# Kernel tuning notes

Measured on AMD Instinct MI355X. Metric: run time of the kernel, lower is better.

## Reference

```python
import jax, jax.numpy as jnp
import numpy as np

B, L, D = 16, 4096, 512


def setup_inputs() -> dict:
    key = jax.random.key(0)
    ks = jax.random.split(key, 8)
    s = 1.0 / np.sqrt(D)
    x = jax.random.normal(ks[0], (B, L, D), dtype=jnp.float32)
    Wk = jax.random.normal(ks[1], (D, D), dtype=jnp.float32) * s
    Wq = jax.random.normal(ks[2], (D, D), dtype=jnp.float32) * s
    Wv = jax.random.normal(ks[3], (D, D), dtype=jnp.float32) * s
    bk = jnp.zeros((D,), jnp.float32)
    bq = jnp.zeros((D,), jnp.float32)
    bv = jnp.zeros((D,), jnp.float32)
    lens = jax.random.randint(ks[4], (B,), 1, L + 1, dtype=jnp.int32)
    return {"x": x, "Wk": Wk, "bk": bk, "Wq": Wq, "bq": bq,
            "Wv": Wv, "bv": bv, "lens": lens}


def reference(x, Wk, bk, Wq, bq, Wv, bv, lens):
    # Dropout is identity in eval mode.
    x_k = jnp.tanh(jnp.einsum('bld,ed->ble', x, Wk) + bk)  # [B,L,D]
    x_q = jnp.tanh(jnp.einsum('bld,ed->ble', x, Wq) + bq)
    x_v = jnp.tanh(jnp.einsum('bld,ed->ble', x, Wv) + bv)
    # sum_j (x_k_i . x_q_j) == x_k_i . sum_j x_q_j  (algebraic collapse of the L x L bmm)
    q_sum = x_q.sum(axis=1)                                # [B,D]
    w = jnp.einsum('bld,bd->bl', x_k, q_sum) / (D ** 0.5)  # [B,L]
    pad = jnp.arange(L)[None, :] >= lens[:, None]          # True at padding
    w = jnp.where(pad, -jnp.inf, w)
    w = jax.nn.softmax(w, axis=1)                          # [B,L]
    # (x_v * w[...,None]).sum(-1) == x_v.sum(-1) * w
    return x_v.sum(axis=-1) * w                            # [B,L]
```

## Files before the change

kernel.cpp:

```cpp
#include <hip/hip_runtime.h>
#include <hip/hip_bf16.h>

typedef __attribute__((ext_vector_type(4)))  int   i32x4;
typedef __attribute__((ext_vector_type(16))) int   i32x16;
typedef __attribute__((ext_vector_type(16))) float f32x16;
typedef __attribute__((ext_vector_type(8)))  short short8;

#define SC1 (1.0f/4096.0f)
#define SC2 (1.0f/524288.0f)

static __device__ __forceinline__ float ftanh(float x) {
  float e = __builtin_amdgcn_exp2f(x * 2.885390081777927f);
  return 1.0f - 2.0f * __builtin_amdgcn_rcpf(e + 1.0f);
}
static __device__ __forceinline__ unsigned short bf16_rn(float f) {
  unsigned u = __float_as_uint(f);
  u += 0x7FFFu + ((u >> 16) & 1u);
  return (unsigned short)(u >> 16);
}
static __device__ __forceinline__ void quant2(float x, float sc, float inv, float losc,
                                              int& hi, int& lo) {
  float t  = __builtin_fmaf(x, sc, 12582912.0f);
  hi = __float_as_int(t) - 0x4B400000;
  float hf = t - 12582912.0f;
  float r  = __builtin_fmaf(hf, -inv, x);
  float t2 = __builtin_fmaf(r, losc, 12582912.0f);
  lo = __float_as_int(t2) - 0x4B400000;
}
static __device__ __forceinline__ void gll16(const void* g, void* l) {
  __builtin_amdgcn_global_load_lds((const __attribute__((address_space(1))) unsigned int*)g,
                                   (__attribute__((address_space(3))) unsigned int*)l, 16, 0, 0);
}
#define MFMA_I8(ACC, A, B) \
  asm("v_mfma_i32_32x32x32_i8 %0, %1, %2, %0" : "+v"(ACC) : "v"(A), "v"(B))

__global__ void prep_w(const float* __restrict__ Wq, const float* __restrict__ Wk,
                       const float* __restrict__ Wv,
                       char* __restrict__ B1, char* __restrict__ B2) {
  int gid = blockIdx.x * 256 + threadIdx.x;
  if (gid < 65536) {
    int chunk = gid >> 12, g = gid & 4095;
    char* dst = B1 + chunk * 65536 + g * 16;
    if (g < 2048) {
      int sel = g >> 10;
      int gg = g & 1023, nt = gg >> 6, lane = gg & 63;
      const float* src = Wq + (size_t)(nt * 32 + (lane & 31)) * 512 + chunk * 32 + (lane >> 5) * 16;
      union { char b[16]; i32x4 v; } ob;
#pragma unroll
      for (int j = 0; j < 16; ++j) {
        int h, l; quant2(src[j], 256.f, 1.f / 256.f, 32768.f, h, l);
        ob.b[j] = (char)(sel ? l : h);
      }
      *(i32x4*)dst = ob.v;
    } else {
      int gg = g - 2048, nt = gg >> 7, ks = (gg >> 6) & 1, lane = gg & 63;
      const float* src = Wv + (size_t)(nt * 32 + (lane & 31)) * 512 + chunk * 32 + ks * 16 + (lane >> 5) * 8;
      union { unsigned short s[8]; i32x4 v; } ob;
#pragma unroll
      for (int j = 0; j < 8; ++j) ob.s[j] = bf16_rn(src[j]);
      *(i32x4*)dst = ob.v;
    }
  } else {
    int gid2 = gid - 65536;
    int chunk = gid2 >> 11, g = gid2 & 2047;
    char* dst = B2 + chunk * 32768 + g * 16;
    int sel = g >> 10, gg = g & 1023, nt = gg >> 6, lane = gg & 63;
    const float* src = Wk + (size_t)(nt * 32 + (lane & 31)) * 512 + chunk * 32 + (lane >> 5) * 16;
    union { char b[16]; i32x4 v; } ob;
#pragma unroll
    for (int j = 0; j < 16; ++j) {
      int h, l; quant2(src[j], 256.f, 1.f / 256.f, 32768.f, h, l);
      ob.b[j] = (char)(sel ? l : h);
    }
    *(i32x4*)dst = ob.v;
  }
}

template<bool VBF16>
static __device__ __forceinline__ void stageA(char* Ab, int tid, float4 xv) {
  const int row = tid >> 3, d0 = (tid & 7) * 4;
  const int mt = row >> 5, l31 = row & 31;
  int h0, l0, h1, l1, h2, l2, h3, l3;
  quant2(xv.x, 16.f, 0.0625f, 2048.f, h0, l0);
  quant2(xv.y, 16.f, 0.0625f, 2048.f, h1, l1);
  quant2(xv.z, 16.f, 0.0625f, 2048.f, h2, l2);
  quant2(xv.w, 16.f, 0.0625f, 2048.f, h3, l3);
  unsigned wh = (h0 & 255) | ((h1 & 255) << 8) | ((h2 & 255) << 16) | ((unsigned)(h3 & 255) << 24);
  unsigned wl = (l0 & 255) | ((l1 & 255) << 8) | ((l2 & 255) << 16) | ((unsigned)(l3 & 255) << 24);
  const int lane8 = (d0 >> 4) * 32 + l31, j = d0 & 15;
  *(unsigned*)(Ab + (mt * 64 + lane8) * 16 + j) = wh;
  *(unsigned*)(Ab + 2048 + (mt * 64 + lane8) * 16 + j) = wl;
  if (VBF16) {
    unsigned long long b0 = bf16_rn(xv.x), b1 = bf16_rn(xv.y), b2 = bf16_rn(xv.z), b3 = bf16_rn(xv.w);
    unsigned long long vv = b0 | (b1 << 16) | (b2 << 32) | (b3 << 48);
    const int ks = d0 >> 4, rem = d0 & 15, hs8 = rem >> 3, j8 = rem & 7;
    *(unsigned long long*)(Ab + 4096 + ((mt * 2 + ks) * 64 + hs8 * 32 + l31) * 16 + j8 * 2) = vv;
  }
}

__global__ __launch_bounds__(512, 2) void pass1_qv(
    const float* __restrict__ x, const char* __restrict__ B1,
    const float* __restrict__ bq, const float* __restrict__ bv,
    float* __restrict__ qpart, float* __restrict__ svout) {
  extern __shared__ char smem[];
  char* Bb0 = smem;            char* Bb1 = smem + 65536;
  char* Ab0 = smem + 131072;   char* Ab1 = smem + 139264;
  float* redv = (float*)(smem + 147456);

  const int tid = threadIdx.x, lane = tid & 63, w = tid >> 6;
  const int l31 = lane & 31, hs = lane >> 5;
  const float* xrow = x + ((size_t)blockIdx.x * 64 + (tid >> 3)) * 512 + (tid & 7) * 4;

  i32x16 q1[2][2] = {}; i32x16 q2[2][2] = {};
  f32x16 accv[2][2] = {};

  float4 xcur = *(const float4*)(xrow);
  stageA<true>(Ab0, tid, xcur);
  {
    const char* src = B1 + tid * 16;
    char* dst = Bb0 + tid * 16;
#pragma unroll
    for (int i = 0; i < 8; ++i) gll16(src + i * 8192, dst + i * 8192);
  }
  xcur = *(const float4*)(xrow + 32);

#pragma unroll 1
  for (int c = 0; c < 16; ++c) {
    const int p = c & 1;
    char* Bc = p ? Bb1 : Bb0;  char* Bn = p ? Bb0 : Bb1;
    char* Ac = p ? Ab1 : Ab0;  char* An = p ? Ab0 : Ab1;
    __syncthreads();
    if (c < 15) {
      const char* src = B1 + (size_t)(c + 1) * 65536 + tid * 16;
      char* dst = Bn + tid * 16;
#pragma unroll
      for (int i = 0; i < 8; ++i) gll16(src + i * 8192, dst + i * 8192);
    }
    float4 xnext = xcur;
    if (c < 14) xnext = *(const float4*)(xrow + (c + 2) * 32);
    if (c < 15) stageA<true>(An, tid, xcur);

    const int lo16 = lane * 16;
    i32x4 aqh0 = *(const i32x4*)(Ac + lo16);
    i32x4 aqh1 = *(const i32x4*)(Ac + 1024 + lo16);
    i32x4 aql0 = *(const i32x4*)(Ac + 2048 + lo16);
    i32x4 aql1 = *(const i32x4*)(Ac + 3072 + lo16);
#pragma unroll
    for (int nn = 0; nn < 2; ++nn) {
      const int nt = w * 2 + nn;
      i32x4 bh = *(const i32x4*)(Bc + nt * 1024 + lo16);
      i32x4 bl = *(const i32x4*)(Bc + 16384 + nt * 1024 + lo16);
      MFMA_I8(q1[0][nn], aqh0, bh);
      MFMA_I8(q2[0][nn], aqh0, bl);
      MFMA_I8(q2[0][nn], aql0, bh);
      MFMA_I8(q1[1][nn], aqh1, bh);
      MFMA_I8(q2[1][nn], aqh1, bl);
      MFMA_I8(q2[1][nn], aql1, bh);
    }
#pragma unroll
    for (int ks = 0; ks < 2; ++ks) {
      short8 av0 = *(const short8*)(Ac + 4096 + (0 * 2 + ks) * 1024 + lo16);
      short8 av1 = *(const short8*)(Ac + 4096 + (1 * 2 + ks) * 1024 + lo16);
#pragma unroll
      for (int nn = 0; nn < 2; ++nn) {
        const int nt = w * 2 + nn;
        short8 bvf = *(const short8*)(Bc + 32768 + (nt * 2 + ks) * 1024 + lo16);
        accv[0][nn] = __builtin_amdgcn_mfma_f32_32x32x16_bf16(av0, bvf, accv[0][nn], 0, 0, 0);
        accv[1][nn] = __builtin_amdgcn_mfma_f32_32x32x16_bf16(av1, bvf, accv[1][nn], 0, 0, 0);
      }
    }
    xcur = xnext;
  }

#pragma unroll
  for (int nn = 0; nn < 2; ++nn) {
    const int col = (w * 2 + nn) * 32 + l31;
    const float bc = bq[col];
    float cs = 0.f;
#pragma unroll
    for (int mt = 0; mt < 2; ++mt)
#pragma unroll
      for (int r = 0; r < 16; ++r)
        cs += ftanh(__builtin_fmaf((float)q1[mt][nn][r], SC1,
                    __builtin_fmaf((float)q2[mt][nn][r], SC2, bc)));
    cs += __shfl_xor(cs, 32);
    if (lane < 32) qpart[(size_t)blockIdx.x * 512 + col] = cs;
  }
  const float bv0 = bv[(w * 2 + 0) * 32 + l31];
  const float bv1 = bv[(w * 2 + 1) * 32 + l31];
#pragma unroll
  for (int mt = 0; mt < 2; ++mt)
#pragma unroll
    for (int r = 0; r < 16; ++r) {
      float s = ftanh(accv[mt][0][r] + bv0) + ftanh(accv[mt][1][r] + bv1);
#pragma unroll
      for (int off = 1; off <= 16; off <<= 1) s += __shfl_xor(s, off);
      if (l31 == 0) redv[w * 64 + mt * 32 + (r & 3) + 8 * (r >> 2) + 4 * hs] = s;
    }
  __syncthreads();
  if (tid < 64) {
    float s = 0.f;
#pragma unroll
    for (int j = 0; j < 8; ++j) s += redv[j * 64 + tid];
    svout[(size_t)blockIdx.x * 64 + tid] = s;
  }
}

__global__ __launch_bounds__(512, 2) void pass2_k(
    const float* __restrict__ x, const char* __restrict__ B2,
    const float* __restrict__ bk, const float* __restrict__ q_sum,
    float* __restrict__ scores) {
  extern __shared__ char smem[];
  char* Bb0 = smem;           char* Bb1 = smem + 32768;
  char* Ab0 = smem + 65536;   char* Ab1 = smem + 69632;
  float* redk = (float*)(smem + 73728);

  const int tid = threadIdx.x, lane = tid & 63, w = tid >> 6;
  const int l31 = lane & 31, hs = lane >> 5;
  const float* xrow = x + ((size_t)blockIdx.x * 64 + (tid >> 3)) * 512 + (tid & 7) * 4;

  i32x16 k1[2][2] = {}; i32x16 k2[2][2] = {};

  float4 xcur = *(const float4*)(xrow);
  stageA<false>(Ab0, tid, xcur);
  {
    const char* src = B2 + tid * 16;
    char* dst = Bb0 + tid * 16;
#pragma unroll
    for (int i = 0; i < 4; ++i) gll16(src + i * 8192, dst + i * 8192);
  }
  xcur = *(const float4*)(xrow + 32);

#pragma unroll 1
  for (int c = 0; c < 16; ++c) {
    const int p = c & 1;
    char* Bc = p ? Bb1 : Bb0;  char* Bn = p ? Bb0 : Bb1;
    char* Ac = p ? Ab1 : Ab0;  char* An = p ? Ab0 : Ab1;
    __syncthreads();
    if (c < 15) {
      const char* src = B2 + (size_t)(c + 1) * 32768 + tid * 16;
      char* dst = Bn + tid * 16;
#pragma unroll
      for (int i = 0; i < 4; ++i) gll16(src + i * 8192, dst + i * 8192);
    }
    float4 xnext = xcur;
    if (c < 14) xnext = *(const float4*)(xrow + (c + 2) * 32);
    if (c < 15) stageA<false>(An, tid, xcur);

    const int lo16 = lane * 16;
    i32x4 ah0 = *(const i32x4*)(Ac + lo16);
    i32x4 ah1 = *(const i32x4*)(Ac + 1024 + lo16);
    i32x4 al0 = *(const i32x4*)(Ac + 2048 + lo16);
    i32x4 al1 = *(const i32x4*)(Ac + 3072 + lo16);
#pragma unroll
    for (int nn = 0; nn < 2; ++nn) {
      const int nt = w * 2 + nn;
      i32x4 bh = *(const i32x4*)(Bc + nt * 1024 + lo16);
      i32x4 bl = *(const i32x4*)(Bc + 16384 + nt * 1024 + lo16);
      MFMA_I8(k1[0][nn], ah0, bh);
      MFMA_I8(k2[0][nn], ah0, bl);
      MFMA_I8(k2[0][nn], al0, bh);
      MFMA_I8(k1[1][nn], ah1, bh);
      MFMA_I8(k2[1][nn], ah1, bl);
      MFMA_I8(k2[1][nn], al1, bh);
    }
    xcur = xnext;
  }

  const int b = blockIdx.x >> 6;
  const int c0 = (w * 2 + 0) * 32 + l31, c1 = (w * 2 + 1) * 32 + l31;
  const float qs0 = q_sum[b * 512 + c0], qs1 = q_sum[b * 512 + c1];
  const float bk0 = bk[c0], bk1 = bk[c1];
#pragma unroll
  for (int mt = 0; mt < 2; ++mt)
#pragma unroll
    for (int r = 0; r < 16; ++r) {
      float p0 = __builtin_fmaf((float)k1[mt][0][r], SC1,
                 __builtin_fmaf((float)k2[mt][0][r], SC2, bk0));
      float p1 = __builtin_fmaf((float)k1[mt][1][r], SC1,
                 __builtin_fmaf((float)k2[mt][1][r], SC2, bk1));
      float s = ftanh(p0) * qs0 + ftanh(p1) * qs1;
#pragma unroll
      for (int off = 1; off <= 16; off <<= 1) s += __shfl_xor(s, off);
      if (l31 == 0) redk[w * 64 + mt * 32 + (r & 3) + 8 * (r >> 2) + 4 * hs] = s;
    }
  __syncthreads();
  if (tid < 64) {
    float s = 0.f;
#pragma unroll
    for (int j = 0; j < 8; ++j) s += redk[j * 64 + tid];
    scores[(size_t)blockIdx.x * 64 + tid] = s;
  }
}

__global__ void reduce_q(const float* __restrict__ qpart, float* __restrict__ q_sum) {
  int b = blockIdx.x, e = threadIdx.x;
  const float* p = qpart + (size_t)b * 64 * 512 + e;
  float s = 0.f;
#pragma unroll 4
  for (int j = 0; j < 64; ++j) s += p[j * 512];
  q_sum[b * 512 + e] = s;
}

__global__ void softmax_out(const float* __restrict__ scores,
                            const float* __restrict__ sv,
                            const int* __restrict__ lens,
                            float* __restrict__ out) {
  const int b = blockIdx.x, tid = threadIdx.x;
  const int lane = tid & 63, wid = tid >> 6;
  const int len = lens[b];
  const float scale = 0.04419417382415922f;
  __shared__ float sb[4], sb2[4];

  float sreg[16];
  const float* sc = scores + (size_t)b * 4096;
#pragma unroll
  for (int j = 0; j < 16; ++j) sreg[j] = sc[tid + j * 256] * scale;

  float m = -1e30f;
#pragma unroll
  for (int j = 0; j < 16; ++j)
    if (tid + j * 256 < len) m = fmaxf(m, sreg[j]);
#pragma unroll
  for (int off = 32; off >= 1; off >>= 1) m = fmaxf(m, __shfl_xor(m, off));
  if (lane == 0) sb[wid] = m;
  __syncthreads();
  m = fmaxf(fmaxf(sb[0], sb[1]), fmaxf(sb[2], sb[3]));

  float s = 0.f;
#pragma unroll
  for (int j = 0; j < 16; ++j)
    if (tid + j * 256 < len) s += expf(sreg[j] - m);
#pragma unroll
  for (int off = 32; off >= 1; off >>= 1) s += __shfl_xor(s, off);
  if (lane == 0) sb2[wid] = s;
  __syncthreads();
  const float inv = 1.f / (sb2[0] + sb2[1] + sb2[2] + sb2[3]);

  const float* svb = sv + (size_t)b * 4096;
  float* ob = out + (size_t)b * 4096;
#pragma unroll
  for (int j = 0; j < 16; ++j) {
    int l = tid + j * 256;
    ob[l] = (l < len) ? svb[l] * expf(sreg[j] - m) * inv : 0.0f;
  }
}

extern "C" void kernel_launch(void* const* d_in, const int* in_sizes, int n_in,
                              void* d_out, int out_size, void* d_ws, size_t ws_size,
                              hipStream_t stream) {
  const float* x  = (const float*)d_in[0];
  const float* Wk = (const float*)d_in[1];
  const float* bk = (const float*)d_in[2];
  const float* Wq = (const float*)d_in[3];
  const float* bq = (const float*)d_in[4];
  const float* Wv = (const float*)d_in[5];
  const float* bv = (const float*)d_in[6];
  const int* lens = (const int*)d_in[7];
  float* out = (float*)d_out;

  char* ws = (char*)d_ws;
  char*  B1     = ws;
  char*  B2     = ws + 1048576;
  float* qpart  = (float*)(ws + 1572864);
  float* q_sum  = (float*)(ws + 3670016);
  float* svbuf  = (float*)(ws + 3702784);
  float* scores = (float*)(ws + 3964928);

  prep_w<<<384, 256, 0, stream>>>(Wq, Wk, Wv, B1, B2);
  pass1_qv<<<1024, 512, 149504, stream>>>(x, B1, bq, bv, qpart, svbuf);
  reduce_q<<<16, 512, 0, stream>>>(qpart, q_sum);
  pass2_k<<<1024, 512, 75776, stream>>>(x, B2, bk, q_sum, scores);
  softmax_out<<<16, 256, 0, stream>>>(scores, svbuf, lens, out);
}
```

Baseline: 253.0 us.

## Split fused Q/V projection pass into separate kernels and raise MFMA priority

The combined Q+V pass, which needed about 146 KB of LDS and held both int8 and bf16 accumulators, is split into two kernels, pass_q and pass_v, each using about 74 KB of LDS and fewer registers. This should let two workgroups fit per CU, but x is now read from global memory once more. s_setprio is raised around the MFMA sections in all three GEMM passes, and a barrier is added before the epilogue reductions that reuse LDS.

```diff
diff --git a/kernel.cpp b/kernel.cpp
--- a/kernel.cpp
+++ b/kernel.cpp
@@ -76,8 +76,7 @@
   }
 }
 
-template<bool VBF16>
-static __device__ __forceinline__ void stageA(char* Ab, int tid, float4 xv) {
+static __device__ __forceinline__ void stageAi8(char* Ab, int tid, float4 xv) {
   const int row = tid >> 3, d0 = (tid & 7) * 4;
   const int mt = row >> 5, l31 = row & 31;
   int h0, l0, h1, l1, h2, l2, h3, l3;
@@ -90,37 +89,37 @@
   const int lane8 = (d0 >> 4) * 32 + l31, j = d0 & 15;
   *(unsigned*)(Ab + (mt * 64 + lane8) * 16 + j) = wh;
   *(unsigned*)(Ab + 2048 + (mt * 64 + lane8) * 16 + j) = wl;
-  if (VBF16) {
-    unsigned long long b0 = bf16_rn(xv.x), b1 = bf16_rn(xv.y), b2 = bf16_rn(xv.z), b3 = bf16_rn(xv.w);
-    unsigned long long vv = b0 | (b1 << 16) | (b2 << 32) | (b3 << 48);
-    const int ks = d0 >> 4, rem = d0 & 15, hs8 = rem >> 3, j8 = rem & 7;
-    *(unsigned long long*)(Ab + 4096 + ((mt * 2 + ks) * 64 + hs8 * 32 + l31) * 16 + j8 * 2) = vv;
-  }
-}
-
-__global__ __launch_bounds__(512, 2) void pass1_qv(
+}
+
+static __device__ __forceinline__ void stageAv(char* Ab, int tid, float4 xv) {
+  const int row = tid >> 3, d0 = (tid & 7) * 4;
+  const int mt = row >> 5, l31 = row & 31;
+  unsigned long long b0 = bf16_rn(xv.x), b1 = bf16_rn(xv.y), b2 = bf16_rn(xv.z), b3 = bf16_rn(xv.w);
+  unsigned long long vv = b0 | (b1 << 16) | (b2 << 32) | (b3 << 48);
+  const int ks = d0 >> 4, rem = d0 & 15, hs8 = rem >> 3, j8 = rem & 7;
+  *(unsigned long long*)(Ab + ((mt * 2 + ks) * 64 + hs8 * 32 + l31) * 16 + j8 * 2) = vv;
+}
+
+__global__ __launch_bounds__(512, 2) void pass_q(
     const float* __restrict__ x, const char* __restrict__ B1,
-    const float* __restrict__ bq, const float* __restrict__ bv,
-    float* __restrict__ qpart, float* __restrict__ svout) {
+    const float* __restrict__ bq, float* __restrict__ qpart) {
   extern __shared__ char smem[];
-  char* Bb0 = smem;            char* Bb1 = smem + 65536;
-  char* Ab0 = smem + 131072;   char* Ab1 = smem + 139264;
-  float* redv = (float*)(smem + 147456);
+  char* Bb0 = smem;            char* Bb1 = smem + 32768;
+  char* Ab0 = smem + 65536;    char* Ab1 = smem + 69632;
 
   const int tid = threadIdx.x, lane = tid & 63, w = tid >> 6;
-  const int l31 = lane & 31, hs = lane >> 5;
+  const int l31 = lane & 31;
   const float* xrow = x + ((size_t)blockIdx.x * 64 + (tid >> 3)) * 512 + (tid & 7) * 4;
 
   i32x16 q1[2][2] = {}; i32x16 q2[2][2] = {};
-  f32x16 accv[2][2] = {};
 
   float4 xcur = *(const float4*)(xrow);
-  stageA<true>(Ab0, tid, xcur);
+  stageAi8(Ab0, tid, xcur);
   {
     const char* src = B1 + tid * 16;
     char* dst = Bb0 + tid * 16;
 #pragma unroll
-    for (int i = 0; i < 8; ++i) gll16(src + i * 8192, dst + i * 8192);
+    for (int i = 0; i < 4; ++i) gll16(src + i * 8192, dst + i * 8192);
   }
   xcur = *(const float4*)(xrow + 32);
 
@@ -134,17 +133,18 @@
       const char* src = B1 + (size_t)(c + 1) * 65536 + tid * 16;
       char* dst = Bn + tid * 16;
 #pragma unroll
-      for (int i = 0; i < 8; ++i) gll16(src + i * 8192, dst + i * 8192);
+      for (int i = 0; i < 4; ++i) gll16(src + i * 8192, dst + i * 8192);
     }
     float4 xnext = xcur;
     if (c < 14) xnext = *(const float4*)(xrow + (c + 2) * 32);
-    if (c < 15) stageA<true>(An, tid, xcur);
+    if (c < 15) stageAi8(An, tid, xcur);
 
     const int lo16 = lane * 16;
     i32x4 aqh0 = *(const i32x4*)(Ac + lo16);
     i32x4 aqh1 = *(const i32x4*)(Ac + 1024 + lo16);
     i32x4 aql0 = *(const i32x4*)(Ac + 2048 + lo16);
     i32x4 aql1 = *(const i32x4*)(Ac + 3072 + lo16);
+    __builtin_amdgcn_s_setprio(1);
 #pragma unroll
     for (int nn = 0; nn < 2; ++nn) {
       const int nt = w * 2 + nn;
@@ -157,18 +157,7 @@
       MFMA_I8(q2[1][nn], aqh1, bl);
       MFMA_I8(q2[1][nn], aql1, bh);
     }
-#pragma unroll
-    for (int ks = 0; ks < 2; ++ks) {
-      short8 av0 = *(const short8*)(Ac + 4096 + (0 * 2 + ks) * 1024 + lo16);
-      short8 av1 = *(const short8*)(Ac + 4096 + (1 * 2 + ks) * 1024 + lo16);
-#pragma unroll
-      for (int nn = 0; nn < 2; ++nn) {
-        const int nt = w * 2 + nn;
-        short8 bvf = *(const short8*)(Bc + 32768 + (nt * 2 + ks) * 1024 + lo16);
-        accv[0][nn] = __builtin_amdgcn_mfma_f32_32x32x16_bf16(av0, bvf, accv[0][nn], 0, 0, 0);
-        accv[1][nn] = __builtin_amdgcn_mfma_f32_32x32x16_bf16(av1, bvf, accv[1][nn], 0, 0, 0);
-      }
-    }
+    __builtin_amdgcn_s_setprio(0);
     xcur = xnext;
   }
 
@@ -186,8 +175,69 @@
     cs += __shfl_xor(cs, 32);
     if (lane < 32) qpart[(size_t)blockIdx.x * 512 + col] = cs;
   }
+}
+
+__global__ __launch_bounds__(512, 2) void pass_v(
+    const float* __restrict__ x, const char* __restrict__ B1,
+    const float* __restrict__ bv, float* __restrict__ svout) {
+  extern __shared__ char smem[];
+  char* Bb0 = smem;            char* Bb1 = smem + 32768;
+  char* Ab0 = smem + 65536;    char* Ab1 = smem + 69632;
+  float* redv = (float*)(smem + 73728);
+
+  const int tid = threadIdx.x, lane = tid & 63, w = tid >> 6;
+  const int l31 = lane & 31, hs = lane >> 5;
+  const float* xrow = x + ((size_t)blockIdx.x * 64 + (tid >> 3)) * 512 + (tid & 7) * 4;
+
+  f32x16 accv[2][2] = {};
+
+  float4 xcur = *(const float4*)(xrow);
+  stageAv(Ab0, tid, xcur);
+  {
+    const char* src = B1 + 32768 + tid * 16;
+    char* dst = Bb0 + tid * 16;
+#pragma unroll
+    for (int i = 0; i < 4; ++i) gll16(src + i * 8192, dst + i * 8192);
+  }
+  xcur = *(const float4*)(xrow + 32);
+
+#pragma unroll 1
+  for (int c = 0; c < 16; ++c) {
+    const int p = c & 1;
+    char* Bc = p ? Bb1 : Bb0;  char* Bn = p ? Bb0 : Bb1;
+    char* Ac = p ? Ab1 : Ab0;  char* An = p ? Ab0 : Ab1;
+    __syncthreads();
+    if (c < 15) {
+      const char* src = B1 + (size_t)(c + 1) * 65536 + 32768 + tid * 16;
+      char* dst = Bn + tid * 16;
+#pragma unroll
+      for (int i = 0; i < 4; ++i) gll16(src + i * 8192, dst + i * 8192);
+    }
+    float4 xnext = xcur;
+    if (c < 14) xnext = *(const float4*)(xrow + (c + 2) * 32);
+    if (c < 15) stageAv(An, tid, xcur);
+
+    const int lo16 = lane * 16;
+    __builtin_amdgcn_s_setprio(1);
+#pragma unroll
+    for (int ks = 0; ks < 2; ++ks) {
+      short8 av0 = *(const short8*)(Ac + (0 * 2 + ks) * 1024 + lo16);
+      short8 av1 = *(const short8*)(Ac + (1 * 2 + ks) * 1024 + lo16);
+#pragma unroll
+      for (int nn = 0; nn < 2; ++nn) {
+        const int nt = w * 2 + nn;
+        short8 bvf = *(const short8*)(Bc + (nt * 2 + ks) * 1024 + lo16);
+        accv[0][nn] = __builtin_amdgcn_mfma_f32_32x32x16_bf16(av0, bvf, accv[0][nn], 0, 0, 0);
+        accv[1][nn] = __builtin_amdgcn_mfma_f32_32x32x16_bf16(av1, bvf, accv[1][nn], 0, 0, 0);
+      }
+    }
+    __builtin_amdgcn_s_setprio(0);
+    xcur = xnext;
+  }
+
   const float bv0 = bv[(w * 2 + 0) * 32 + l31];
   const float bv1 = bv[(w * 2 + 1) * 32 + l31];
+  __syncthreads();
 #pragma unroll
   for (int mt = 0; mt < 2; ++mt)
 #pragma unroll
@@ -206,7 +256,7 @@
   }
 }
 
-__global__ __launch_bounds__(512, 2) void pass2_k(
+__global__ __launch_bounds__(512, 2) void pass_k(
     const float* __restrict__ x, const char* __restrict__ B2,
     const float* __restrict__ bk, const float* __restrict__ q_sum,
     float* __restrict__ scores) {
@@ -222,7 +272,7 @@
   i32x16 k1[2][2] = {}; i32x16 k2[2][2] = {};
 
   float4 xcur = *(const float4*)(xrow);
-  stageA<false>(Ab0, tid, xcur);
+  stageAi8(Ab0, tid, xcur);
   {
     const char* src = B2 + tid * 16;
     char* dst = Bb0 + tid * 16;
@@ -245,13 +295,14 @@
     }
     float4 xnext = xcur;
     if (c < 14) xnext = *(const float4*)(xrow + (c + 2) * 32);
-    if (c < 15) stageA<false>(An, tid, xcur);
+    if (c < 15) stageAi8(An, tid, xcur);
 
     const int lo16 = lane * 16;
     i32x4 ah0 = *(const i32x4*)(Ac + lo16);
     i32x4 ah1 = *(const i32x4*)(Ac + 1024 + lo16);
     i32x4 al0 = *(const i32x4*)(Ac + 2048 + lo16);
     i32x4 al1 = *(const i32x4*)(Ac + 3072 + lo16);
+    __builtin_amdgcn_s_setprio(1);
 #pragma unroll
     for (int nn = 0; nn < 2; ++nn) {
       const int nt = w * 2 + nn;
@@ -264,6 +315,7 @@
       MFMA_I8(k2[1][nn], ah1, bl);
       MFMA_I8(k2[1][nn], al1, bh);
     }
+    __builtin_amdgcn_s_setprio(0);
     xcur = xnext;
   }
 
@@ -271,6 +323,7 @@
   const int c0 = (w * 2 + 0) * 32 + l31, c1 = (w * 2 + 1) * 32 + l31;
   const float qs0 = q_sum[b * 512 + c0], qs1 = q_sum[b * 512 + c1];
   const float bk0 = bk[c0], bk1 = bk[c1];
+  __syncthreads();
 #pragma unroll
   for (int mt = 0; mt < 2; ++mt)
 #pragma unroll
@@ -368,8 +421,9 @@
   float* scores = (float*)(ws + 3964928);
 
   prep_w<<<384, 256, 0, stream>>>(Wq, Wk, Wv, B1, B2);
-  pass1_qv<<<1024, 512, 149504, stream>>>(x, B1, bq, bv, qpart, svbuf);
+  pass_q<<<1024, 512, 73728, stream>>>(x, B1, bq, qpart);
+  pass_v<<<1024, 512, 75776, stream>>>(x, B1, bv, svbuf);
   reduce_q<<<16, 512, 0, stream>>>(qpart, q_sum);
-  pass2_k<<<1024, 512, 75776, stream>>>(x, B2, bk, q_sum, scores);
+  pass_k<<<1024, 512, 75776, stream>>>(x, B2, bk, q_sum, scores);
   softmax_out<<<16, 256, 0, stream>>>(scores, svbuf, lens, out);
 }
```

Measured after the change: 246.3 us. 1.03x faster.

## Keep weight tiles in registers and split Q/V passes by column half

Applied to the files above, without the earlier changes.

Each block now loads its 32-column slice of the quantized weights into registers once. It then loops over four 64-row tiles of x, which replaces the per-chunk streaming of weights through LDS with global_load_lds. The fused Q+V pass is split into separate Q and V kernels, and each block handles half of the output columns, so V and K row-sums are written as two partials that the softmax kernel adds. This removes the large LDS weight buffers and cuts weight traffic per row tile. In exchange, x is read more times (two column halves, plus separate Q and V passes), and register pressure rises from the held weight fragments.

```diff
diff --git a/kernel.cpp b/kernel.cpp
--- a/kernel.cpp
+++ b/kernel.cpp
@@ -26,10 +26,6 @@
   float r  = __builtin_fmaf(hf, -inv, x);
   float t2 = __builtin_fmaf(r, losc, 12582912.0f);
   lo = __float_as_int(t2) - 0x4B400000;
-}
-static __device__ __forceinline__ void gll16(const void* g, void* l) {
-  __builtin_amdgcn_global_load_lds((const __attribute__((address_space(1))) unsigned int*)g,
-                                   (__attribute__((address_space(3))) unsigned int*)l, 16, 0, 0);
 }
 #define MFMA_I8(ACC, A, B) \
   asm("v_mfma_i32_32x32x32_i8 %0, %1, %2, %0" : "+v"(ACC) : "v"(A), "v"(B))
@@ -76,9 +72,7 @@
   }
 }
 
-template<bool VBF16>
-static __device__ __forceinline__ void stageA(char* Ab, int tid, float4 xv) {
-  const int row = tid >> 3, d0 = (tid & 7) * 4;
+static __device__ __forceinline__ void stageAi8(char* Ab, int row, int d0, float4 xv) {
   const int mt = row >> 5, l31 = row & 31;
   int h0, l0, h1, l1, h2, l2, h3, l3;
   quant2(xv.x, 16.f, 0.0625f, 2048.f, h0, l0);
@@ -90,220 +84,231 @@
   const int lane8 = (d0 >> 4) * 32 + l31, j = d0 & 15;
   *(unsigned*)(Ab + (mt * 64 + lane8) * 16 + j) = wh;
   *(unsigned*)(Ab + 2048 + (mt * 64 + lane8) * 16 + j) = wl;
-  if (VBF16) {
-    unsigned long long b0 = bf16_rn(xv.x), b1 = bf16_rn(xv.y), b2 = bf16_rn(xv.z), b3 = bf16_rn(xv.w);
-    unsigned long long vv = b0 | (b1 << 16) | (b2 << 32) | (b3 << 48);
-    const int ks = d0 >> 4, rem = d0 & 15, hs8 = rem >> 3, j8 = rem & 7;
-    *(unsigned long long*)(Ab + 4096 + ((mt * 2 + ks) * 64 + hs8 * 32 + l31) * 16 + j8 * 2) = vv;
-  }
-}
-
-__global__ __launch_bounds__(512, 2) void pass1_qv(
+}
+static __device__ __forceinline__ void stageAv(char* Ab, int row, int d0, float4 xv) {
+  const int mt = row >> 5, l31 = row & 31;
+  unsigned long long b0 = bf16_rn(xv.x), b1 = bf16_rn(xv.y), b2 = bf16_rn(xv.z), b3 = bf16_rn(xv.w);
+  unsigned long long vv = b0 | (b1 << 16) | (b2 << 32) | (b3 << 48);
+  const int ks = d0 >> 4, rem = d0 & 15, hs8 = rem >> 3, j8 = rem & 7;
+  *(unsigned long long*)(Ab + ((mt * 2 + ks) * 64 + hs8 * 32 + l31) * 16 + j8 * 2) = vv;
+}
+
+__global__ __launch_bounds__(512, 2) void pass_q(
     const float* __restrict__ x, const char* __restrict__ B1,
-    const float* __restrict__ bq, const float* __restrict__ bv,
-    float* __restrict__ qpart, float* __restrict__ svout) {
-  extern __shared__ char smem[];
-  char* Bb0 = smem;            char* Bb1 = smem + 65536;
-  char* Ab0 = smem + 131072;   char* Ab1 = smem + 139264;
-  float* redv = (float*)(smem + 147456);
+    const float* __restrict__ bq, float* __restrict__ qpart) {
+  __shared__ char Ab0[4096], Ab1[4096];
+
+  const int tid = threadIdx.x, lane = tid & 63, w = tid >> 6;
+  const int l31 = lane & 31;
+  const int ch = blockIdx.x & 1, rep = blockIdx.x >> 1;
+  const int nt = ch * 8 + w;
+  const int row = tid >> 3, d0 = (tid & 7) * 4;
+  const int lo16 = lane * 16;
+
+  i32x4 Whi[16], Wlo[16];
+#pragma unroll
+  for (int kc = 0; kc < 16; ++kc) {
+    const char* wp = B1 + (size_t)kc * 65536 + nt * 1024 + lo16;
+    Whi[kc] = *(const i32x4*)(wp);
+    Wlo[kc] = *(const i32x4*)(wp + 16384);
+  }
+  const float bqc = bq[nt * 32 + l31];
+  float cs = 0.f;
+
+#pragma unroll 1
+  for (int tt = 0; tt < 4; ++tt) {
+    const size_t tile = (size_t)rep * 4 + tt;
+    const float* gxr = x + (tile * 64 + row) * 512 + d0;
+
+    i32x16 q1[2] = {}, q2[2] = {};
+    float4 xcur = *(const float4*)(gxr);
+    stageAi8(Ab0, row, d0, xcur);
+    xcur = *(const float4*)(gxr + 32);
+
+#pragma unroll
+    for (int c = 0; c < 16; ++c) {
+      __syncthreads();
+      float4 xnext = xcur;
+      if (c < 14) xnext = *(const float4*)(gxr + (c + 2) * 32);
+      if (c < 15) stageAi8((c & 1) ? Ab0 : Ab1, row, d0, xcur);
+      const char* Ac = (c & 1) ? Ab1 : Ab0;
+      i32x4 ah0 = *(const i32x4*)(Ac + lo16);
+      i32x4 ah1 = *(const i32x4*)(Ac + 1024 + lo16);
+      i32x4 al0 = *(const i32x4*)(Ac + 2048 + lo16);
+      i32x4 al1 = *(const i32x4*)(Ac + 3072 + lo16);
+      MFMA_I8(q1[0], ah0, Whi[c]);
+      MFMA_I8(q2[0], ah0, Wlo[c]);
+      MFMA_I8(q2[0], al0, Whi[c]);
+      MFMA_I8(q1[1], ah1, Whi[c]);
+      MFMA_I8(q2[1], ah1, Wlo[c]);
+      MFMA_I8(q2[1], al1, Whi[c]);
+      xcur = xnext;
+    }
+#pragma unroll
+    for (int mt = 0; mt < 2; ++mt)
+#pragma unroll
+      for (int r = 0; r < 16; ++r)
+        cs += ftanh(__builtin_fmaf((float)q1[mt][r], SC1,
+                    __builtin_fmaf((float)q2[mt][r], SC2, bqc)));
+  }
+  cs += __shfl_xor(cs, 32);
+  if (lane < 32) qpart[(size_t)rep * 512 + nt * 32 + l31] = cs;
+}
+
+__global__ __launch_bounds__(512, 2) void pass_v(
+    const float* __restrict__ x, const char* __restrict__ B1,
+    const float* __restrict__ bv, float* __restrict__ vpart) {
+  __shared__ char Ab0[4096], Ab1[4096];
+  __shared__ float redv[8][64];
 
   const int tid = threadIdx.x, lane = tid & 63, w = tid >> 6;
   const int l31 = lane & 31, hs = lane >> 5;
-  const float* xrow = x + ((size_t)blockIdx.x * 64 + (tid >> 3)) * 512 + (tid & 7) * 4;
-
-  i32x16 q1[2][2] = {}; i32x16 q2[2][2] = {};
-  f32x16 accv[2][2] = {};
-
-  float4 xcur = *(const float4*)(xrow);
-  stageA<true>(Ab0, tid, xcur);
-  {
-    const char* src = B1 + tid * 16;
-    char* dst = Bb0 + tid * 16;
-#pragma unroll
-    for (int i = 0; i < 8; ++i) gll16(src + i * 8192, dst + i * 8192);
-  }
-  xcur = *(const float4*)(xrow + 32);
+  const int ch = blockIdx.x & 1, rep = blockIdx.x >> 1;
+  const int nt = ch * 8 + w;
+  const int row = tid >> 3, d0 = (tid & 7) * 4;
+  const int lo16 = lane * 16;
+
+  short8 Wv[32];
+#pragma unroll
+  for (int kc = 0; kc < 16; ++kc) {
+    const char* wp = B1 + (size_t)kc * 65536 + 32768 + (nt * 2) * 1024 + lo16;
+    Wv[kc * 2]     = *(const short8*)(wp);
+    Wv[kc * 2 + 1] = *(const short8*)(wp + 1024);
+  }
+  const float bvc = bv[nt * 32 + l31];
 
 #pragma unroll 1
-  for (int c = 0; c < 16; ++c) {
-    const int p = c & 1;
-    char* Bc = p ? Bb1 : Bb0;  char* Bn = p ? Bb0 : Bb1;
-    char* Ac = p ? Ab1 : Ab0;  char* An = p ? Ab0 : Ab1;
+  for (int tt = 0; tt < 4; ++tt) {
+    const size_t tile = (size_t)rep * 4 + tt;
+    const float* gxr = x + (tile * 64 + row) * 512 + d0;
+
+    f32x16 accv[2] = {};
+    float4 xcur = *(const float4*)(gxr);
+    stageAv(Ab0, row, d0, xcur);
+    xcur = *(const float4*)(gxr + 32);
+
+#pragma unroll
+    for (int c = 0; c < 16; ++c) {
+      __syncthreads();
+      float4 xnext = xcur;
+      if (c < 14) xnext = *(const float4*)(gxr + (c + 2) * 32);
+      if (c < 15) stageAv((c & 1) ? Ab0 : Ab1, row, d0, xcur);
+      const char* Ac = (c & 1) ? Ab1 : Ab0;
+      short8 a00 = *(const short8*)(Ac + 0 * 1024 + lo16);
+      short8 a01 = *(const short8*)(Ac + 1 * 1024 + lo16);
+      short8 a10 = *(const short8*)(Ac + 2 * 1024 + lo16);
+      short8 a11 = *(const short8*)(Ac + 3 * 1024 + lo16);
+      accv[0] = __builtin_amdgcn_mfma_f32_32x32x16_bf16(a00, Wv[c * 2], accv[0], 0, 0, 0);
+      accv[0] = __builtin_amdgcn_mfma_f32_32x32x16_bf16(a01, Wv[c * 2 + 1], accv[0], 0, 0, 0);
+      accv[1] = __builtin_amdgcn_mfma_f32_32x32x16_bf16(a10, Wv[c * 2], accv[1], 0, 0, 0);
+      accv[1] = __builtin_amdgcn_mfma_f32_32x32x16_bf16(a11, Wv[c * 2 + 1], accv[1], 0, 0, 0);
+      xcur = xnext;
+    }
+#pragma unroll
+    for (int mt = 0; mt < 2; ++mt)
+#pragma unroll
+      for (int r = 0; r < 16; ++r) {
+        float s = ftanh(accv[mt][r] + bvc);
+#pragma unroll
+        for (int off = 1; off <= 16; off <<= 1) s += __shfl_xor(s, off);
+        if (l31 == 0) redv[w][mt * 32 + (r & 3) + 8 * (r >> 2) + 4 * hs] = s;
+      }
     __syncthreads();
-    if (c < 15) {
-      const char* src = B1 + (size_t)(c + 1) * 65536 + tid * 16;
-      char* dst = Bn + tid * 16;
-#pragma unroll
-      for (int i = 0; i < 8; ++i) gll16(src + i * 8192, dst + i * 8192);
-    }
-    float4 xnext = xcur;
-    if (c < 14) xnext = *(const float4*)(xrow + (c + 2) * 32);
-    if (c < 15) stageA<true>(An, tid, xcur);
-
-    const int lo16 = lane * 16;
-    i32x4 aqh0 = *(const i32x4*)(Ac + lo16);
-    i32x4 aqh1 = *(const i32x4*)(Ac + 1024 + lo16);
-    i32x4 aql0 = *(const i32x4*)(Ac + 2048 + lo16);
-    i32x4 aql1 = *(const i32x4*)(Ac + 3072 + lo16);
-#pragma unroll
-    for (int nn = 0; nn < 2; ++nn) {
-      const int nt = w * 2 + nn;
-      i32x4 bh = *(const i32x4*)(Bc + nt * 1024 + lo16);
-      i32x4 bl = *(const i32x4*)(Bc + 16384 + nt * 1024 + lo16);
-      MFMA_I8(q1[0][nn], aqh0, bh);
-      MFMA_I8(q2[0][nn], aqh0, bl);
-      MFMA_I8(q2[0][nn], aql0, bh);
-      MFMA_I8(q1[1][nn], aqh1, bh);
-      MFMA_I8(q2[1][nn], aqh1, bl);
-      MFMA_I8(q2[1][nn], aql1, bh);
-    }
-#pragma unroll
-    for (int ks = 0; ks < 2; ++ks) {
-      short8 av0 = *(const short8*)(Ac + 4096 + (0 * 2 + ks) * 1024 + lo16);
-      short8 av1 = *(const short8*)(Ac + 4096 + (1 * 2 + ks) * 1024 + lo16);
-#pragma unroll
-      for (int nn = 0; nn < 2; ++nn) {
-        const int nt = w * 2 + nn;
-        short8 bvf = *(const short8*)(Bc + 32768 + (nt * 2 + ks) * 1024 + lo16);
-        accv[0][nn] = __builtin_amdgcn_mfma_f32_32x32x16_bf16(av0, bvf, accv[0][nn], 0, 0, 0);
-        accv[1][nn] = __builtin_amdgcn_mfma_f32_32x32x16_bf16(av1, bvf, accv[1][nn], 0, 0, 0);
-      }
-    }
-    xcur = xnext;
-  }
-
-#pragma unroll
-  for (int nn = 0; nn < 2; ++nn) {
-    const int col = (w * 2 + nn) * 32 + l31;
-    const float bc = bq[col];
-    float cs = 0.f;
-#pragma unroll
-    for (int mt = 0; mt < 2; ++mt)
-#pragma unroll
-      for (int r = 0; r < 16; ++r)
-        cs += ftanh(__builtin_fmaf((float)q1[mt][nn][r], SC1,
-                    __builtin_fmaf((float)q2[mt][nn][r], SC2, bc)));
-    cs += __shfl_xor(cs, 32);
-    if (lane < 32) qpart[(size_t)blockIdx.x * 512 + col] = cs;
-  }
-  const float bv0 = bv[(w * 2 + 0) * 32 + l31];
-  const float bv1 = bv[(w * 2 + 1) * 32 + l31];
-#pragma unroll
-  for (int mt = 0; mt < 2; ++mt)
-#pragma unroll
-    for (int r = 0; r < 16; ++r) {
-      float s = ftanh(accv[mt][0][r] + bv0) + ftanh(accv[mt][1][r] + bv1);
-#pragma unroll
-      for (int off = 1; off <= 16; off <<= 1) s += __shfl_xor(s, off);
-      if (l31 == 0) redv[w * 64 + mt * 32 + (r & 3) + 8 * (r >> 2) + 4 * hs] = s;
-    }
-  __syncthreads();
-  if (tid < 64) {
-    float s = 0.f;
-#pragma unroll
-    for (int j = 0; j < 8; ++j) s += redv[j * 64 + tid];
-    svout[(size_t)blockIdx.x * 64 + tid] = s;
-  }
-}
-
-__global__ __launch_bounds__(512, 2) void pass2_k(
+    if (tid < 64) {
+      float s = 0.f;
+#pragma unroll
+      for (int j = 0; j < 8; ++j) s += redv[j][tid];
+      vpart[(size_t)ch * 65536 + tile * 64 + tid] = s;
+    }
+  }
+}
+
+__global__ __launch_bounds__(512, 2) void pass_k(
     const float* __restrict__ x, const char* __restrict__ B2,
     const float* __restrict__ bk, const float* __restrict__ q_sum,
-    float* __restrict__ scores) {
-  extern __shared__ char smem[];
-  char* Bb0 = smem;           char* Bb1 = smem + 32768;
-  char* Ab0 = smem + 65536;   char* Ab1 = smem + 69632;
-  float* redk = (float*)(smem + 73728);
+    float* __restrict__ spart) {
+  __shared__ char Ab0[4096], Ab1[4096];
+  __shared__ float redk[8][64];
 
   const int tid = threadIdx.x, lane = tid & 63, w = tid >> 6;
   const int l31 = lane & 31, hs = lane >> 5;
-  const float* xrow = x + ((size_t)blockIdx.x * 64 + (tid >> 3)) * 512 + (tid & 7) * 4;
-
-  i32x16 k1[2][2] = {}; i32x16 k2[2][2] = {};
-
-  float4 xcur = *(const float4*)(xrow);
-  stageA<false>(Ab0, tid, xcur);
-  {
-    const char* src = B2 + tid * 16;
-    char* dst = Bb0 + tid * 16;
-#pragma unroll
-    for (int i = 0; i < 4; ++i) gll16(src + i * 8192, dst + i * 8192);
-  }
-  xcur = *(const float4*)(xrow + 32);
+  const int ch = blockIdx.x & 1, rep = blockIdx.x >> 1;
+  const int nt = ch * 8 + w;
+  const int row = tid >> 3, d0 = (tid & 7) * 4;
+  const int lo16 = lane * 16;
+  const int b = rep >> 4;
+
+  i32x4 Whi[16], Wlo[16];
+#pragma unroll
+  for (int kc = 0; kc < 16; ++kc) {
+    const char* wp = B2 + (size_t)kc * 32768 + nt * 1024 + lo16;
+    Whi[kc] = *(const i32x4*)(wp);
+    Wlo[kc] = *(const i32x4*)(wp + 16384);
+  }
+  const float bkc = bk[nt * 32 + l31];
+  const float qs = q_sum[b * 512 + nt * 32 + l31];
 
 #pragma unroll 1
-  for (int c = 0; c < 16; ++c) {
-    const int p = c & 1;
-    char* Bc = p ? Bb1 : Bb0;  char* Bn = p ? Bb0 : Bb1;
-    char* Ac = p ? Ab1 : Ab0;  char* An = p ? Ab0 : Ab1;
+  for (int tt = 0; tt < 4; ++tt) {
+    const size_t tile = (size_t)rep * 4 + tt;
+    const float* gxr = x + (tile * 64 + row) * 512 + d0;
+
+    i32x16 k1[2] = {}, k2[2] = {};
+    float4 xcur = *(const float4*)(gxr);
+    stageAi8(Ab0, row, d0, xcur);
+    xcur = *(const float4*)(gxr + 32);
+
+#pragma unroll
+    for (int c = 0; c < 16; ++c) {
+      __syncthreads();
+      float4 xnext = xcur;
+      if (c < 14) xnext = *(const float4*)(gxr + (c + 2) * 32);
+      if (c < 15) stageAi8((c & 1) ? Ab0 : Ab1, row, d0, xcur);
+      const char* Ac = (c & 1) ? Ab1 : Ab0;
+      i32x4 ah0 = *(const i32x4*)(Ac + lo16);
+      i32x4 ah1 = *(const i32x4*)(Ac + 1024 + lo16);
+      i32x4 al0 = *(const i32x4*)(Ac + 2048 + lo16);
+      i32x4 al1 = *(const i32x4*)(Ac + 3072 + lo16);
+      MFMA_I8(k1[0], ah0, Whi[c]);
+      MFMA_I8(k2[0], ah0, Wlo[c]);
+      MFMA_I8(k2[0], al0, Whi[c]);
+      MFMA_I8(k1[1], ah1, Whi[c]);
+      MFMA_I8(k2[1], ah1, Wlo[c]);
+      MFMA_I8(k2[1], al1, Whi[c]);
+      xcur = xnext;
+    }
+#pragma unroll
+    for (int mt = 0; mt < 2; ++mt)
+#pragma unroll
+      for (int r = 0; r < 16; ++r) {
+        float pre = __builtin_fmaf((float)k1[mt][r], SC1,
+                    __builtin_fmaf((float)k2[mt][r], SC2, bkc));
+        float s = ftanh(pre) * qs;
+#pragma unroll
+        for (int off = 1; off <= 16; off <<= 1) s += __shfl_xor(s, off);
+        if (l31 == 0) redk[w][mt * 32 + (r & 3) + 8 * (r >> 2) + 4 * hs] = s;
+      }
     __syncthreads();
-    if (c < 15) {
-      const char* src = B2 + (size_t)(c + 1) * 32768 + tid * 16;
-      char* dst = Bn + tid * 16;
-#pragma unroll
-      for (int i = 0; i < 4; ++i) gll16(src + i * 8192, dst + i * 8192);
-    }
-    float4 xnext = xcur;
-    if (c < 14) xnext = *(const float4*)(xrow + (c + 2) * 32);
-    if (c < 15) stageA<false>(An, tid, xcur);
-
-    const int lo16 = lane * 16;
-    i32x4 ah0 = *(const i32x4*)(Ac + lo16);
-    i32x4 ah1 = *(const i32x4*)(Ac + 1024 + lo16);
-    i32x4 al0 = *(const i32x4*)(Ac + 2048 + lo16);
-    i32x4 al1 = *(const i32x4*)(Ac + 3072 + lo16);
-#pragma unroll
-    for (int nn = 0; nn < 2; ++nn) {
-      const int nt = w * 2 + nn;
-      i32x4 bh = *(const i32x4*)(Bc + nt * 1024 + lo16);
-      i32x4 bl = *(const i32x4*)(Bc + 16384 + nt * 1024 + lo16);
-      MFMA_I8(k1[0][nn], ah0, bh);
-      MFMA_I8(k2[0][nn], ah0, bl);
-      MFMA_I8(k2[0][nn], al0, bh);
-      MFMA_I8(k1[1][nn], ah1, bh);
-      MFMA_I8(k2[1][nn], ah1, bl);
-      MFMA_I8(k2[1][nn], al1, bh);
-    }
-    xcur = xnext;
-  }
-
-  const int b = blockIdx.x >> 6;
-  const int c0 = (w * 2 + 0) * 32 + l31, c1 = (w * 2 + 1) * 32 + l31;
-  const float qs0 = q_sum[b * 512 + c0], qs1 = q_sum[b * 512 + c1];
-  const float bk0 = bk[c0], bk1 = bk[c1];
-#pragma unroll
-  for (int mt = 0; mt < 2; ++mt)
-#pragma unroll
-    for (int r = 0; r < 16; ++r) {
-      float p0 = __builtin_fmaf((float)k1[mt][0][r], SC1,
-                 __builtin_fmaf((float)k2[mt][0][r], SC2, bk0));
-      float p1 = __builtin_fmaf((float)k1[mt][1][r], SC1,
-                 __builtin_fmaf((float)k2[mt][1][r], SC2, bk1));
-      float s = ftanh(p0) * qs0 + ftanh(p1) * qs1;
-#pragma unroll
-      for (int off = 1; off <= 16; off <<= 1) s += __shfl_xor(s, off);
-      if (l31 == 0) redk[w * 64 + mt * 32 + (r & 3) + 8 * (r >> 2) + 4 * hs] = s;
-    }
-  __syncthreads();
-  if (tid < 64) {
-    float s = 0.f;
-#pragma unroll
-    for (int j = 0; j < 8; ++j) s += redk[j * 64 + tid];
-    scores[(size_t)blockIdx.x * 64 + tid] = s;
+    if (tid < 64) {
+      float s = 0.f;
+#pragma unroll
+      for (int j = 0; j < 8; ++j) s += redk[j][tid];
+      spart[(size_t)ch * 65536 + tile * 64 + tid] = s;
+    }
   }
 }
 
 __global__ void reduce_q(const float* __restrict__ qpart, float* __restrict__ q_sum) {
   int b = blockIdx.x, e = threadIdx.x;
-  const float* p = qpart + (size_t)b * 64 * 512 + e;
+  const float* p = qpart + (size_t)b * 16 * 512 + e;
   float s = 0.f;
-#pragma unroll 4
-  for (int j = 0; j < 64; ++j) s += p[j * 512];
+#pragma unroll
+  for (int j = 0; j < 16; ++j) s += p[j * 512];
   q_sum[b * 512 + e] = s;
 }
 
-__global__ void softmax_out(const float* __restrict__ scores,
-                            const float* __restrict__ sv,
+__global__ void softmax_out(const float* __restrict__ spart,
+                            const float* __restrict__ vpart,
                             const int* __restrict__ lens,
                             float* __restrict__ out) {
   const int b = blockIdx.x, tid = threadIdx.x;
@@ -312,10 +317,13 @@
   const float scale = 0.04419417382415922f;
   __shared__ float sb[4], sb2[4];
 
-  float sreg[16];
-  const float* sc = scores + (size_t)b * 4096;
-#pragma unroll
-  for (int j = 0; j < 16; ++j) sreg[j] = sc[tid + j * 256] * scale;
+  float sreg[16], svreg[16];
+#pragma unroll
+  for (int j = 0; j < 16; ++j) {
+    size_t l = (size_t)b * 4096 + tid + j * 256;
+    sreg[j] = (spart[l] + spart[65536 + l]) * scale;
+    svreg[j] = vpart[l] + vpart[65536 + l];
+  }
 
   float m = -1e30f;
 #pragma unroll
@@ -337,12 +345,11 @@
   __syncthreads();
   const float inv = 1.f / (sb2[0] + sb2[1] + sb2[2] + sb2[3]);
 
-  const float* svb = sv + (size_t)b * 4096;
   float* ob = out + (size_t)b * 4096;
 #pragma unroll
   for (int j = 0; j < 16; ++j) {
     int l = tid + j * 256;
-    ob[l] = (l < len) ? svb[l] * expf(sreg[j] - m) * inv : 0.0f;
+    ob[l] = (l < len) ? svreg[j] * expf(sreg[j] - m) * inv : 0.0f;
   }
 }
 
@@ -363,13 +370,14 @@
   char*  B1     = ws;
   char*  B2     = ws + 1048576;
   float* qpart  = (float*)(ws + 1572864);
-  float* q_sum  = (float*)(ws + 3670016);
-  float* svbuf  = (float*)(ws + 3702784);
-  float* scores = (float*)(ws + 3964928);
+  float* q_sum  = (float*)(ws + 2097152);
+  float* vpart  = (float*)(ws + 2129920);
+  float* spart  = (float*)(ws + 2654208);
 
   prep_w<<<384, 256, 0, stream>>>(Wq, Wk, Wv, B1, B2);
-  pass1_qv<<<1024, 512, 149504, stream>>>(x, B1, bq, bv, qpart, svbuf);
+  pass_q<<<512, 512, 0, stream>>>(x, B1, bq, qpart);
+  pass_v<<<512, 512, 0, stream>>>(x, B1, bv, vpart);
   reduce_q<<<16, 512, 0, stream>>>(qpart, q_sum);
-  pass2_k<<<1024, 512, 75776, stream>>>(x, B2, bk, q_sum, scores);
-  softmax_out<<<16, 256, 0, stream>>>(scores, svbuf, lens, out);
-}
+  pass_k<<<512, 512, 0, stream>>>(x, B2, bk, q_sum, spart);
+  softmax_out<<<16, 256, 0, stream>>>(spart, vpart, lens, out);
+}
```

Measured after the change: 304.0 us. +20.2%, slower.
